# Kernel tuning notes

Hardware: AMD Instinct MI355X
Metric: run time of the kernel (lower is better)

## Reference

```python
import jax, jax.numpy as jnp
import numpy as np

B, T, S, CD = 256, 512, 8, 4          # batch, max seq len, state_dim, control_dim
RNN = 512                              # control_rnn_size
H = RNN + S                            # LSTM hidden = 520
E = 2 * RNN                            # encoder hidden (encoder_size * x_dnn_osz)
D = 2 * H                              # decoder hidden (decoder_size * u_dnn_isz)


def setup_inputs() -> dict:
    key = jax.random.key(0)
    ks = jax.random.split(key, 16)
    g = lambda k, shp, s=0.05: jax.random.normal(k, shp, dtype=jnp.float32) * s
    return {
        "x": g(ks[0], (B, S), 1.0),
        "rnn_input": g(ks[1], (B, T, CD + 1), 1.0),
        "deltas": jax.random.uniform(ks[2], (B, T, 1), dtype=jnp.float32),
        "h_lens": jax.random.randint(ks[3], (B,), 1, T + 1),
        "enc_w1": g(ks[4], (S, E)), "enc_b1": jnp.zeros((E,), jnp.float32),
        "enc_w2": g(ks[5], (E, E)), "enc_b2": jnp.zeros((E,), jnp.float32),
        "enc_w3": g(ks[6], (E, RNN)), "enc_b3": jnp.zeros((RNN,), jnp.float32),
        "W_ih": g(ks[7], (CD + 1, 4 * H)), "W_hh": g(ks[8], (H, 4 * H)),
        "b_lstm": jnp.zeros((4 * H,), jnp.float32),
        "dec_w1": g(ks[9], (H, D)), "dec_b1": jnp.zeros((D,), jnp.float32),
        "dec_w2": g(ks[10], (D, D)), "dec_b2": jnp.zeros((D,), jnp.float32),
        "dec_w3": g(ks[11], (D, S)), "dec_b3": jnp.zeros((S,), jnp.float32),
    }


def reference(x, rnn_input, deltas, h_lens,
              enc_w1, enc_b1, enc_w2, enc_b2, enc_w3, enc_b3,
              W_ih, W_hh, b_lstm,
              dec_w1, dec_b1, dec_w2, dec_b2, dec_w3, dec_b3):
    # ---- encoder (FFNet with Tanh, final linear) ----
    h0 = jnp.tanh(x @ enc_w1 + enc_b1)
    h0 = jnp.tanh(h0 @ enc_w2 + enc_b2)
    h0 = h0 @ enc_w3 + enc_b3                       # [B, RNN]
    h0_stack = jnp.concatenate([x, h0], axis=1)     # [B, H]
    c0 = jnp.zeros_like(h0_stack)

    # ---- packed-sequence LSTM scan (state frozen / output zero past h_lens) ----
    u_seq = jnp.transpose(rnn_input, (1, 0, 2))     # [T, B, CD+1]
    t_idx = jnp.arange(rnn_input.shape[1])

    def step(carry, inps):
        h, c = carry
        u_t, t = inps
        gates = u_t @ W_ih + h @ W_hh + b_lstm      # [B, 4H], torch gate order i,f,g,o
        i, f, g_, o = jnp.split(gates, 4, axis=-1)
        c_new = jax.nn.sigmoid(f) * c + jax.nn.sigmoid(i) * jnp.tanh(g_)
        h_new = jax.nn.sigmoid(o) * jnp.tanh(c_new)
        valid = (t < h_lens)[:, None]
        h_k = jnp.where(valid, h_new, h)
        c_k = jnp.where(valid, c_new, c)
        y = jnp.where(valid, h_new, 0.0)            # pad_packed pads with zeros
        return (h_k, c_k), y

    _, ys = jax.lax.scan(step, (h0_stack, c0), (u_seq, t_idx))
    h_seq = jnp.transpose(ys, (1, 0, 2))            # [B, T, H]

    # ---- roll-shift + convex blend with deltas ----
    h_shift = jnp.roll(h_seq, 1, axis=1).at[:, 0, :].set(h0_stack)
    encoded = (1.0 - deltas) * h_shift + deltas * h_seq

    # ---- variable-length gather at h_lens-1, then decoder MLP ----
    last = encoded[jnp.arange(encoded.shape[0]), h_lens - 1, :]  # [B, H]
    z = jnp.tanh(last @ dec_w1 + dec_b1)
    z = jnp.tanh(z @ dec_w2 + dec_b2)
    out = z @ dec_w3 + dec_b3
    return out[:, :S]
```

## Files before the change

kernel.cpp:

```cpp
#include <hip/hip_runtime.h>
#include <math.h>

#define Bz   256
#define Tz   512
#define Sz   8
#define CD1  5
#define Hz   520
#define H4   2080
#define Ez   1024
#define Dz   1040

#define NG   16
#define NSL  16
#define RG   16
#define JW   34
#define NW   136
#define KW   520
#define KD   260
#define KIT  17
#define HGTQ 4160
#define NTHR 512

typedef float f32x4 __attribute__((ext_vector_type(4)));
typedef short s16x8 __attribute__((ext_vector_type(8)));
typedef unsigned long long ull;

__device__ __forceinline__ ushort f2bf(float f) {
    uint u = __float_as_uint(f);
    uint r = (u + 0x7fffu + ((u >> 16) & 1u)) >> 16;
    return (ushort)r;
}
__device__ __forceinline__ float bf2f(ushort h) { return __uint_as_float(((uint)h) << 16); }
__device__ __forceinline__ float sigf(float v) { return 1.0f / (1.0f + expf(-v)); }

__global__ void k_sort(const int* __restrict__ hl, int* __restrict__ sortedidx) {
    __shared__ int s[Bz];
    int i = threadIdx.x;
    s[i] = hl[i];
    __syncthreads();
    int mine = s[i], rank = 0;
    for (int j = 0; j < Bz; j++) {
        int o = s[j];
        rank += (o > mine) || (o == mine && j < i);
    }
    sortedidx[rank] = i;
}

__global__ void k_prep_w(const float* __restrict__ whh, ushort* __restrict__ wbt) {
    int idx = blockIdx.x * 256 + threadIdx.x;
    if (idx >= NW * NSL * KW) return;
    int n = idx / KW, k = idx - n * KW;
    int j = n >> 2, gate = n & 3;
    float v = (j < Hz) ? whh[(size_t)k * H4 + gate * Hz + j] : 0.0f;
    wbt[idx] = f2bf(v);
}

__global__ void k_hinit(const float* __restrict__ hA, const int* __restrict__ sortedidx,
                        ull* __restrict__ h_buf1) {
    int idx = blockIdx.x * 256 + threadIdx.x;
    if (idx >= Bz * KD) return;
    int rank = idx / KD, kd = idx - rank * KD;
    const float* src = hA + (size_t)sortedidx[rank] * KW + 2 * kd;
    uint lo = 0xFFFF0000u | (uint)f2bf(src[0]);
    uint hi = 0xFFFF0000u | (uint)f2bf(src[1]);
    h_buf1[idx] = (ull)lo | ((ull)hi << 32);
}

template<int K, int N, int ACT>
__global__ void k_mlp(const float* __restrict__ in, const float* __restrict__ w,
                      const float* __restrict__ bias, float* __restrict__ out) {
    int n  = blockIdx.x * 256 + threadIdx.x;
    int m0 = blockIdx.y * 4;
    if (n >= N) return;
    float acc[4];
    float bv = bias[n];
    #pragma unroll
    for (int i = 0; i < 4; i++) acc[i] = bv;
    for (int k = 0; k < K; k++) {
        float wv = w[k * N + n];
        #pragma unroll
        for (int i = 0; i < 4; i++) acc[i] += in[(m0 + i) * K + k] * wv;
    }
    #pragma unroll
    for (int i = 0; i < 4; i++) {
        float v = acc[i];
        out[(m0 + i) * N + n] = ACT ? tanhf(v) : v;
    }
}

__global__ void k_enc3(const float* __restrict__ h2, const float* __restrict__ w,
                       const float* __restrict__ bias, const float* __restrict__ x,
                       float* __restrict__ hstack) {
    int n  = blockIdx.x * 256 + threadIdx.x;
    int m0 = blockIdx.y * 4;
    float acc[4];
    float bv = bias[n];
    #pragma unroll
    for (int i = 0; i < 4; i++) acc[i] = bv;
    for (int k = 0; k < Ez; k++) {
        float wv = w[k * 512 + n];
        #pragma unroll
        for (int i = 0; i < 4; i++) acc[i] += h2[(m0 + i) * Ez + k] * wv;
    }
    #pragma unroll
    for (int i = 0; i < 4; i++) hstack[(m0 + i) * Hz + Sz + n] = acc[i];
    if (blockIdx.x == 0 && threadIdx.x < Sz) {
        #pragma unroll
        for (int i = 0; i < 4; i++)
            hstack[(m0 + i) * Hz + threadIdx.x] = x[(m0 + i) * Sz + threadIdx.x];
    }
}

__global__ __launch_bounds__(NTHR, 2) void k_lstm(
        const ushort* __restrict__ wbt, const float* __restrict__ rnn_in,
        const float* __restrict__ deltas, const int* __restrict__ h_lens,
        const float* __restrict__ W_ih, const float* __restrict__ b_lstm,
        ull* h_global, const int* __restrict__ sortedidx,
        float* __restrict__ last) {
    __shared__ __align__(16) ushort a_lds[RG * KW];
    __shared__ __align__(16) float  gates_lds[RG * NW];
    __shared__ float c_lds[RG * JW];
    __shared__ int   rowg[RG];
    __shared__ int   hl_s[RG];

    const int tid = threadIdx.x;
    const int bid = blockIdx.x;
    const int g   = (bid & 7) | ((bid >> 7) << 3);
    const int s   = (bid >> 3) & 15;

    if (tid < RG) {
        int o = sortedidx[g * RG + tid];
        rowg[tid] = o;
        hl_s[tid] = h_lens[o];
    }
    for (int idx = tid; idx < RG * JW; idx += NTHR) c_lds[idx] = 0.0f;
    __syncthreads();

    const int lane = tid & 63, wvi = tid >> 6;
    const int l15 = lane & 15, quad = lane >> 4;
    const int ntile = (wvi == 0) ? 2 : 1;
    const int tiles[2] = { wvi, 8 };

    int myrows[4];
    #pragma unroll
    for (int r = 0; r < 4; r++) myrows[r] = rowg[quad * 4 + r];
    const int gmax = hl_s[0];

    s16x8 bfrag[2][KIT];
    #pragma unroll
    for (int i = 0; i < 2; i++) {
        int nl = tiles[i] * 16 + l15;
        bool okrow = (i < ntile) && (nl < NW);
        const uint* wrow = (const uint*)wbt + (size_t)(s * NW + (nl < NW ? nl : 0)) * KD;
        #pragma unroll
        for (int kit = 0; kit < KIT; kit++) {
            s16x8 z = {0, 0, 0, 0, 0, 0, 0, 0};
            if (okrow && (kit * 32 + quad * 8 < KW))
                z = __builtin_bit_cast(s16x8, *(const uint4*)(wrow + kit * 16 + quad * 4));
            bfrag[i][kit] = z;
        }
    }

    float wihreg[2][CD1], breg[2];
    #pragma unroll
    for (int i = 0; i < 2; i++) {
        int nl = tiles[i] * 16 + l15;
        int jg = s * JW + (nl >> 2);
        bool ok = (i < ntile) && (nl < NW) && (jg < Hz);
        int col = (nl & 3) * Hz + (jg < Hz ? jg : 0);
        breg[i] = ok ? b_lstm[col] : 0.0f;
        #pragma unroll
        for (int q = 0; q < CD1; q++) wihreg[i][q] = ok ? W_ih[q * H4 + col] : 0.0f;
    }

    ull* hbuf0 = h_global + (size_t)g * RG * KD;
    ull* hbuf1 = h_global + (size_t)Bz * KD + (size_t)g * RG * KD;

    const uint done_init = (tid < HGTQ - 8 * NTHR) ? 0u : 0x100u;

    for (int t = 0; t < gmax; t++) {
        ull* hwq = (t & 1) ? hbuf1 : hbuf0;
        const ull* hrq = (t & 1) ? hbuf0 : hbuf1;

        float uu[4][CD1];
        #pragma unroll
        for (int r = 0; r < 4; r++) {
            const float* up = rnn_in + ((size_t)myrows[r] * Tz + t) * CD1;
            #pragma unroll
            for (int q = 0; q < CD1; q++) uu[r][q] = up[q];
        }
        f32x4 acc[2];
        #pragma unroll
        for (int i = 0; i < 2; i++) {
            #pragma unroll
            for (int r = 0; r < 4; r++) {
                float a0 = breg[i];
                #pragma unroll
                for (int q = 0; q < CD1; q++) a0 += uu[r][q] * wihreg[i][q];
                acc[i][r] = a0;
            }
        }

        {
            const uint want = (uint)((t - 1) & 0xFFFF);
            uint done = done_init;
            for (;;) {
                ull v[9];
                #pragma unroll
                for (int it = 0; it < 9; it++) {
                    int q = tid + it * NTHR;
                    bool act = !((done >> it) & 1u);
                    v[it] = act ? __hip_atomic_load(hrq + q, __ATOMIC_RELAXED,
                                                    __HIP_MEMORY_SCOPE_AGENT)
                                : 0ull;
                }
                #pragma unroll
                for (int it = 0; it < 9; it++) {
                    if (!((done >> it) & 1u)) {
                        int q = tid + it * NTHR;
                        uint lo = (uint)v[it], hi = (uint)(v[it] >> 32);
                        if ((lo >> 16) == want && (hi >> 16) == want) {
                            ((uint*)a_lds)[q] = (lo & 0xFFFFu) | (hi << 16);
                            done |= 1u << it;
                        }
                    }
                }
                if (__syncthreads_and((int)(done == 0x1FFu))) break;
                __builtin_amdgcn_s_sleep(4);
            }
        }

        for (int kit = 0; kit < KIT; kit++) {
            int kq = kit * 32 + quad * 8;
            s16x8 af = {0, 0, 0, 0, 0, 0, 0, 0};
            if (kq < KW)
                af = __builtin_bit_cast(s16x8,
                    *(const uint4*)((const uint*)a_lds + l15 * KD + kit * 16 + quad * 4));
            #pragma unroll
            for (int i = 0; i < 2; i++) {
                if (i >= ntile) break;
                acc[i] = __builtin_amdgcn_mfma_f32_16x16x32_bf16(af, bfrag[i][kit], acc[i], 0, 0, 0);
            }
        }

        #pragma unroll
        for (int i = 0; i < 2; i++) {
            if (i >= ntile) break;
            int nl = tiles[i] * 16 + l15;
            if (nl < NW) {
                #pragma unroll
                for (int r = 0; r < 4; r++) gates_lds[(quad * 4 + r) * NW + nl] = acc[i][r];
            }
        }
        __syncthreads();

        if (tid < RG * (JW / 2)) {
            int m  = tid / (JW / 2), jp = tid - m * (JW / 2);
            int jj = 2 * jp;
            int jglob = s * JW + jj;
            if (jglob < Hz) {
                uint pd = ((const uint*)a_lds)[m * KD + (jglob >> 1)];
                ushort h0b, h1b;
                if (t < hl_s[m]) {
                    float2 c2 = *(float2*)&c_lds[m * JW + jj];
                    const float* gp = &gates_lds[m * NW + jj * 4];
                    float4 gA = *(const float4*)gp;
                    float4 gB = *(const float4*)(gp + 4);
                    float i0 = sigf(gA.x), f0 = sigf(gA.y), g0 = tanhf(gA.z), o0 = sigf(gA.w);
                    float i1 = sigf(gB.x), f1 = sigf(gB.y), g1 = tanhf(gB.z), o1 = sigf(gB.w);
                    float cn0 = f0 * c2.x + i0 * g0;
                    float cn1 = f1 * c2.y + i1 * g1;
                    float hn0 = o0 * tanhf(cn0);
                    float hn1 = o1 * tanhf(cn1);
                    c2.x = cn0; c2.y = cn1;
                    *(float2*)&c_lds[m * JW + jj] = c2;
                    if (t == hl_s[m] - 1) {
                        float hp0 = bf2f((ushort)(pd & 0xFFFFu));
                        float hp1 = bf2f((ushort)(pd >> 16));
                        int orig = rowg[m];
                        float d = deltas[(size_t)orig * Tz + t];
                        last[(size_t)orig * Hz + jglob]     = (1.0f - d) * hp0 + d * hn0;
                        last[(size_t)orig * Hz + jglob + 1] = (1.0f - d) * hp1 + d * hn1;
                    }
                    h0b = f2bf(hn0);
                    h1b = f2bf(hn1);
                } else {
                    h0b = (ushort)(pd & 0xFFFFu);
                    h1b = (ushort)(pd >> 16);
                }
                uint tagw = ((uint)t & 0xFFFFu) << 16;
                ull pk = (ull)(tagw | (uint)h0b) | ((ull)(tagw | (uint)h1b) << 32);
                __hip_atomic_store(hwq + m * KD + (jglob >> 1), pk,
                                   __ATOMIC_RELAXED, __HIP_MEMORY_SCOPE_AGENT);
            }
        }

        __syncthreads();
    }
}

__global__ void k_dec3(const float* __restrict__ z2, const float* __restrict__ w,
                       const float* __restrict__ bias, float* __restrict__ out) {
    int m = blockIdx.x, tid = threadIdx.x;
    float p[8];
    #pragma unroll
    for (int n = 0; n < 8; n++) p[n] = 0.0f;
    for (int k = tid; k < Dz; k += 256) {
        float zv = z2[(size_t)m * Dz + k];
        #pragma unroll
        for (int n = 0; n < 8; n++) p[n] += zv * w[k * 8 + n];
    }
    __shared__ float red[256][8];
    #pragma unroll
    for (int n = 0; n < 8; n++) red[tid][n] = p[n];
    __syncthreads();
    for (int s2 = 128; s2 > 0; s2 >>= 1) {
        if (tid < s2) {
            #pragma unroll
            for (int n = 0; n < 8; n++) red[tid][n] += red[tid + s2][n];
        }
        __syncthreads();
    }
    if (tid < 8) out[m * 8 + tid] = red[0][tid] + bias[tid];
}

extern "C" void kernel_launch(void* const* d_in, const int* in_sizes, int n_in,
                              void* d_out, int out_size, void* d_ws, size_t ws_size,
                              hipStream_t stream) {
    const float* x       = (const float*)d_in[0];
    const float* rnn_inp = (const float*)d_in[1];
    const float* deltas  = (const float*)d_in[2];
    const int*   h_lens  = (const int*)  d_in[3];
    const float* enc_w1  = (const float*)d_in[4];
    const float* enc_b1  = (const float*)d_in[5];
    const float* enc_w2  = (const float*)d_in[6];
    const float* enc_b2  = (const float*)d_in[7];
    const float* enc_w3  = (const float*)d_in[8];
    const float* enc_b3  = (const float*)d_in[9];
    const float* W_ih    = (const float*)d_in[10];
    const float* W_hh    = (const float*)d_in[11];
    const float* b_lstm  = (const float*)d_in[12];
    const float* dec_w1  = (const float*)d_in[13];
    const float* dec_b1  = (const float*)d_in[14];
    const float* dec_w2  = (const float*)d_in[15];
    const float* dec_b2  = (const float*)d_in[16];
    const float* dec_w3  = (const float*)d_in[17];
    const float* dec_b3  = (const float*)d_in[18];
    (void)in_sizes; (void)n_in; (void)out_size; (void)ws_size;

    char* base = (char*)d_ws;
    size_t off = 0;
    auto alloc = [&](size_t bytes) { void* p = base + off; off = (off + bytes + 255) & ~(size_t)255; return p; };
    ushort* wbt      = (ushort*)alloc((size_t)NW * NSL * KW * 2);
    ull*    h_glob   = (ull*)   alloc((size_t)2 * Bz * KD * 8);
    float*  hA       = (float*) alloc((size_t)Bz * KW * 4);
    float*  h1       = (float*) alloc((size_t)Bz * Ez * 4);
    float*  h2       = (float*) alloc((size_t)Bz * Ez * 4);
    float*  lastb    = (float*) alloc((size_t)Bz * Hz * 4);
    float*  z1       = (float*) alloc((size_t)Bz * Dz * 4);
    float*  z2       = (float*) alloc((size_t)Bz * Dz * 4);
    int*    sortedix = (int*)   alloc(Bz * 4);
    float*  outp = (float*)d_out;

    k_sort<<<1, 256, 0, stream>>>(h_lens, sortedix);
    {
        int total = NW * NSL * KW;
        k_prep_w<<<(total + 255) / 256, 256, 0, stream>>>(W_hh, wbt);
    }

    k_mlp<Sz, Ez, 1><<<dim3(4, 64), 256, 0, stream>>>(x,  enc_w1, enc_b1, h1);
    k_mlp<Ez, Ez, 1><<<dim3(4, 64), 256, 0, stream>>>(h1, enc_w2, enc_b2, h2);
    k_enc3<<<dim3(2, 64), 256, 0, stream>>>(h2, enc_w3, enc_b3, x, hA);
    {
        int total = Bz * KD;
        k_hinit<<<(total + 255) / 256, 256, 0, stream>>>(hA, sortedix,
                                                         h_glob + (size_t)Bz * KD);
    }

    {
        void* args[] = { (void*)&wbt, (void*)&rnn_inp, (void*)&deltas, (void*)&h_lens,
                         (void*)&W_ih, (void*)&b_lstm, (void*)&h_glob, (void*)&sortedix,
                         (void*)&lastb };
        hipLaunchCooperativeKernel(reinterpret_cast<void*>(k_lstm), dim3(NG * NSL), dim3(NTHR),
                                   args, 0, stream);
    }

    k_mlp<Hz, Dz, 1><<<dim3(5, 64), 256, 0, stream>>>(lastb, dec_w1, dec_b1, z1);
    k_mlp<Dz, Dz, 1><<<dim3(5, 64), 256, 0, stream>>>(z1,   dec_w2, dec_b2, z2);
    k_dec3<<<Bz, 256, 0, stream>>>(z2, dec_w3, dec_b3, outp);
}
```

Measured before the change: 2.584 ms.

## Do LSTM cell update in registers via lane shuffles, dropping LDS gates round-trip

Computes the LSTM pointwise cell update directly from the MFMA accumulators. Lane shuffles transpose the four gate values so each lane holds i,f,g,o for one (row, unit). The cell state and previous hidden value stay in registers instead of LDS, which removes the gates_lds staging buffer and one __syncthreads per timestep from the serial recurrence. Tagged h values are now written as 32-bit atomic stores per unit instead of packed 64-bit pairs. Launch bounds drop to one block per CU, which allows more registers but less occupancy.

```diff
diff --git a/kernel.cpp b/kernel.cpp
--- a/kernel.cpp
+++ b/kernel.cpp
@@ -111,15 +111,13 @@
     }
 }
 
-__global__ __launch_bounds__(NTHR, 2) void k_lstm(
+__global__ __launch_bounds__(NTHR, 1) void k_lstm(
         const ushort* __restrict__ wbt, const float* __restrict__ rnn_in,
         const float* __restrict__ deltas, const int* __restrict__ h_lens,
         const float* __restrict__ W_ih, const float* __restrict__ b_lstm,
         ull* h_global, const int* __restrict__ sortedidx,
         float* __restrict__ last) {
     __shared__ __align__(16) ushort a_lds[RG * KW];
-    __shared__ __align__(16) float  gates_lds[RG * NW];
-    __shared__ float c_lds[RG * JW];
     __shared__ int   rowg[RG];
     __shared__ int   hl_s[RG];
 
@@ -133,7 +131,6 @@
         rowg[tid] = o;
         hl_s[tid] = h_lens[o];
     }
-    for (int idx = tid; idx < RG * JW; idx += NTHR) c_lds[idx] = 0.0f;
     __syncthreads();
 
     const int lane = tid & 63, wvi = tid >> 6;
@@ -145,6 +142,18 @@
     #pragma unroll
     for (int r = 0; r < 4; r++) myrows[r] = rowg[quad * 4 + r];
     const int gmax = hl_s[0];
+
+    int ju_[2], jg_[2];
+    #pragma unroll
+    for (int i = 0; i < 2; i++) {
+        ju_[i] = tiles[i] * 4 + (l15 >> 2);
+        jg_[i] = s * JW + ju_[i];
+    }
+    const int em   = quad * 4 + (l15 & 3);
+    const int ehl  = hl_s[em];
+    const int eorig = rowg[em];
+    const int ssrc = (lane & 48) | ((l15 & 3) << 2) | (l15 >> 2);
+    const int sm   = quad * 4 + (l15 >> 2);
 
     s16x8 bfrag[2][KIT];
     #pragma unroll
@@ -173,6 +182,9 @@
         for (int q = 0; q < CD1; q++) wihreg[i][q] = ok ? W_ih[q * H4 + col] : 0.0f;
     }
 
+    float c_reg[2] = {0.0f, 0.0f};
+    float hprev[2] = {0.0f, 0.0f};
+
     ull* hbuf0 = h_global + (size_t)g * RG * KD;
     ull* hbuf1 = h_global + (size_t)Bz * KD + (size_t)g * RG * KD;
 
@@ -181,6 +193,7 @@
     for (int t = 0; t < gmax; t++) {
         ull* hwq = (t & 1) ? hbuf1 : hbuf0;
         const ull* hrq = (t & 1) ? hbuf0 : hbuf1;
+        uint* hwd = (uint*)hwq;
 
         float uu[4][CD1];
         #pragma unroll
@@ -230,6 +243,17 @@
             }
         }
 
+        if (t == 0) {
+            #pragma unroll
+            for (int i = 0; i < 2; i++) {
+                if (i >= ntile) break;
+                if (ju_[i] < JW && jg_[i] < Hz) {
+                    uint pd = ((const uint*)a_lds)[em * KD + (jg_[i] >> 1)];
+                    hprev[i] = bf2f((ushort)((jg_[i] & 1) ? (pd >> 16) : (pd & 0xFFFFu)));
+                }
+            }
+        }
+
         for (int kit = 0; kit < KIT; kit++) {
             int kq = kit * 32 + quad * 8;
             s16x8 af = {0, 0, 0, 0, 0, 0, 0, 0};
@@ -243,54 +267,46 @@
             }
         }
 
+        const uint tagw = ((uint)t & 0xFFFFu) << 16;
         #pragma unroll
         for (int i = 0; i < 2; i++) {
             if (i >= ntile) break;
-            int nl = tiles[i] * 16 + l15;
-            if (nl < NW) {
-                #pragma unroll
-                for (int r = 0; r < 4; r++) gates_lds[(quad * 4 + r) * NW + nl] = acc[i][r];
-            }
-        }
-        __syncthreads();
-
-        if (tid < RG * (JW / 2)) {
-            int m  = tid / (JW / 2), jp = tid - m * (JW / 2);
-            int jj = 2 * jp;
-            int jglob = s * JW + jj;
-            if (jglob < Hz) {
-                uint pd = ((const uint*)a_lds)[m * KD + (jglob >> 1)];
-                ushort h0b, h1b;
-                if (t < hl_s[m]) {
-                    float2 c2 = *(float2*)&c_lds[m * JW + jj];
-                    const float* gp = &gates_lds[m * NW + jj * 4];
-                    float4 gA = *(const float4*)gp;
-                    float4 gB = *(const float4*)(gp + 4);
-                    float i0 = sigf(gA.x), f0 = sigf(gA.y), g0 = tanhf(gA.z), o0 = sigf(gA.w);
-                    float i1 = sigf(gB.x), f1 = sigf(gB.y), g1 = tanhf(gB.z), o1 = sigf(gB.w);
-                    float cn0 = f0 * c2.x + i0 * g0;
-                    float cn1 = f1 * c2.y + i1 * g1;
-                    float hn0 = o0 * tanhf(cn0);
-                    float hn1 = o1 * tanhf(cn1);
-                    c2.x = cn0; c2.y = cn1;
-                    *(float2*)&c_lds[m * JW + jj] = c2;
-                    if (t == hl_s[m] - 1) {
-                        float hp0 = bf2f((ushort)(pd & 0xFFFFu));
-                        float hp1 = bf2f((ushort)(pd >> 16));
-                        int orig = rowg[m];
-                        float d = deltas[(size_t)orig * Tz + t];
-                        last[(size_t)orig * Hz + jglob]     = (1.0f - d) * hp0 + d * hn0;
-                        last[(size_t)orig * Hz + jglob + 1] = (1.0f - d) * hp1 + d * hn1;
+            float v0 = acc[i][0], v1 = acc[i][1], v2 = acc[i][2], v3 = acc[i][3];
+            float x;
+            x = __shfl_xor((lane & 1) ? v0 : v1, 1);
+            if (lane & 1) v0 = x; else v1 = x;
+            x = __shfl_xor((lane & 1) ? v2 : v3, 1);
+            if (lane & 1) v2 = x; else v3 = x;
+            x = __shfl_xor((lane & 2) ? v0 : v2, 2);
+            if (lane & 2) v0 = x; else v2 = x;
+            x = __shfl_xor((lane & 2) ? v1 : v3, 2);
+            if (lane & 2) v1 = x; else v3 = x;
+            uint tg = 0u;
+            bool valid = (ju_[i] < JW) && (jg_[i] < Hz);
+            if (valid) {
+                float hnew;
+                if (t < ehl) {
+                    float ig = sigf(v0), fg = sigf(v1), gt = tanhf(v2), og = sigf(v3);
+                    float cn = fg * c_reg[i] + ig * gt;
+                    c_reg[i] = cn;
+                    float hn = og * tanhf(cn);
+                    if (t == ehl - 1) {
+                        float d = deltas[(size_t)eorig * Tz + t];
+                        last[(size_t)eorig * Hz + jg_[i]] = (1.0f - d) * hprev[i] + d * hn;
                     }
-                    h0b = f2bf(hn0);
-                    h1b = f2bf(hn1);
+                    hnew = hn;
                 } else {
-                    h0b = (ushort)(pd & 0xFFFFu);
-                    h1b = (ushort)(pd >> 16);
+                    hnew = hprev[i];
                 }
-                uint tagw = ((uint)t & 0xFFFFu) << 16;
-                ull pk = (ull)(tagw | (uint)h0b) | ((ull)(tagw | (uint)h1b) << 32);
-                __hip_atomic_store(hwq + m * KD + (jglob >> 1), pk,
+                ushort hb = f2bf(hnew);
+                hprev[i] = bf2f(hb);
+                tg = tagw | (uint)hb;
+            }
+            uint tgs = __shfl(tg, ssrc);
+            int ju_s = tiles[i] * 4 + (l15 & 3);
+            int jg_s = s * JW + ju_s;
+            if (ju_s < JW && jg_s < Hz) {
+                __hip_atomic_store(hwd + sm * KW + jg_s, tgs,
                                    __ATOMIC_RELAXED, __HIP_MEMORY_SCOPE_AGENT);
             }
         }
```

New measurement: 4.026 ms. 1.56x slower.
